# Kernel optimization log

Hardware: AMD Instinct MI355X
Metric: run time of the kernel (lower is better)

## Reference

```python
import jax, jax.numpy as jnp
import numpy as np

B, N, S, K, D = 8, 8192, 1024, 32, 64
RADIUS = 0.2
MLP = [64, 64, 128]
C_IN = 3 + D


def _fps(pts):
    # pts: [N,3] -> [S] farthest-point indices (deterministic start at index 0,
    # matching pytorch3d.sample_farthest_points default random_start_point=False)
    def body(carry, _):
        d, last = carry
        dd = jnp.sum((pts - pts[last]) ** 2, axis=-1)
        d = jnp.minimum(d, dd)
        return (d, jnp.argmax(d)), last
    init = (jnp.full((pts.shape[0],), 1e10, pts.dtype), jnp.asarray(0))
    _, idxs = jax.lax.scan(body, init, None, length=S)
    return idxs


def _ball_query(new_xyz, xyz):
    # new_xyz [B,S,3], xyz [B,N,3] -> idx [B,S,K]
    # classic PointNet++ ball query: first K points (by index order) within radius;
    # queries with fewer than K neighbors are padded by replicating the first hit.
    sqr = jnp.sum((new_xyz[:, :, None, :] - xyz[:, None, :, :]) ** 2, axis=-1)  # [B,S,N]
    cand = jnp.where(sqr <= RADIUS ** 2,
                     jnp.arange(N, dtype=jnp.int32)[None, None, :],
                     jnp.int32(N))
    idx = -jax.lax.top_k(-cand, K)[0]  # K smallest valid indices, ascending
    first = idx[..., :1]
    return jnp.where(idx == N, first, idx)


def _gather(arr, idx):
    # arr [B,N,C], idx [B,S,K] -> [B,S,K,C]
    return jax.vmap(lambda a, i: a[i])(arr, idx)


def _forward(xyz, points, attention, w0, b0, w1, b1, w2, b2):
    x = xyz.transpose(0, 2, 1)        # [B,N,3]
    p = points.transpose(0, 2, 1)     # [B,N,D]
    a = attention.transpose(0, 2, 1)  # [B,N,1]
    fps_idx = jax.vmap(_fps)(x)                      # [B,S]
    new_xyz = jax.vmap(lambda q, i: q[i])(x, fps_idx)  # [B,S,3]
    idx = _ball_query(new_xyz, x)                    # [B,S,K]
    g_norm = _gather(x, idx) - new_xyz[:, :, None, :]   # [B,S,K,3]
    feat = jnp.concatenate([g_norm, _gather(p, idx)], axis=-1)  # [B,S,K,3+D]
    new_att = jnp.mean(_gather(a, idx), axis=-2).reshape(x.shape[0], 1, -1)  # [B,1,S]
    # shared MLP (1x1 Conv2d == per-point dense), no BN (bn=False)
    h = jax.nn.relu(jnp.einsum('bskc,oc->bsko', feat, w0) + b0)
    h = jax.nn.relu(jnp.einsum('bskc,oc->bsko', h, w1) + b1)
    h = jax.nn.relu(jnp.einsum('bskc,oc->bsko', h, w2) + b2)
    new_points = jnp.max(h, axis=2)  # max-pool over nsample -> [B,S,C_out]
    return new_xyz.transpose(0, 2, 1), new_points.transpose(0, 2, 1), new_att


def setup_inputs() -> dict:
    key = jax.random.key(0)
    ks = jax.random.split(key, 9)
    xyz = jax.random.uniform(ks[0], (B, 3, N), dtype=jnp.float32)  # unit cube
    points = jax.random.normal(ks[1], (B, D, N), dtype=jnp.float32)
    attention = jax.random.uniform(ks[2], (B, 1, N), dtype=jnp.float32)
    cin = C_IN
    w0 = jax.random.normal(ks[3], (MLP[0], cin), dtype=jnp.float32) / np.sqrt(cin)
    b0 = jnp.zeros((MLP[0],), jnp.float32)
    w1 = jax.random.normal(ks[4], (MLP[1], MLP[0]), dtype=jnp.float32) / np.sqrt(MLP[0])
    b1 = jnp.zeros((MLP[1],), jnp.float32)
    w2 = jax.random.normal(ks[5], (MLP[2], MLP[1]), dtype=jnp.float32) / np.sqrt(MLP[1])
    b2 = jnp.zeros((MLP[2],), jnp.float32)
    return {"xyz": xyz, "points": points, "attention": attention,
            "w0": w0, "b0": b0, "w1": w1, "b1": b1, "w2": w2, "b2": b2}


def reference(xyz, points, attention, w0, b0, w1, b1, w2, b2):
    return _forward(xyz, points, attention, w0, b0, w1, b1, w2, b2)
```

## Files before the change

### kernel.cpp

```cpp
#include <hip/hip_runtime.h>

#define NPTS 8192
#define NSAMP 1024
#define NBATCH 8
#define KNB 32

typedef float f32x2 __attribute__((ext_vector_type(2)));

__device__ __forceinline__ f32x2 pk_add(f32x2 a, f32x2 b) {
  f32x2 d; asm("v_pk_add_f32 %0, %1, %2" : "=v"(d) : "v"(a), "v"(b)); return d;
}
__device__ __forceinline__ f32x2 pk_mul(f32x2 a, f32x2 b) {
  f32x2 d; asm("v_pk_mul_f32 %0, %1, %2" : "=v"(d) : "v"(a), "v"(b)); return d;
}

#define DPP_FMAX_ROUND(v, CTRL)                                                        \
  do {                                                                                 \
    int _b = __float_as_int(v);                                                        \
    int _p = __builtin_amdgcn_update_dpp(_b, _b, CTRL, 0xF, 0xF, false);               \
    (v) = fmaxf((v), __int_as_float(_p));                                              \
  } while (0)

#define DPP_UMIN_ROUND(v, CTRL)                                                        \
  do {                                                                                 \
    unsigned _p = (unsigned)__builtin_amdgcn_update_dpp((int)(v), (int)(v), CTRL,      \
                                                        0xF, 0xF, false);              \
    if (_p < (v)) (v) = _p;                                                            \
  } while (0)

#define DPP_MIN_ROUND(k, CTRL)                                                         \
  do {                                                                                 \
    unsigned _lo = (unsigned)(k), _hi = (unsigned)((k) >> 32);                         \
    unsigned _plo = (unsigned)__builtin_amdgcn_update_dpp((int)_lo, (int)_lo, CTRL,    \
                                                          0xF, 0xF, false);            \
    unsigned _phi = (unsigned)__builtin_amdgcn_update_dpp((int)_hi, (int)_hi, CTRL,    \
                                                          0xF, 0xF, false);            \
    unsigned long long _ok = (((unsigned long long)_phi) << 32) | _plo;                \
    if (_ok < (k)) (k) = _ok;                                                          \
  } while (0)

__device__ __forceinline__ float sqdist_rn(float px, float py, float pz,
                                           float qx, float qy, float qz) {
  float dx = px - qx, dy = py - qy, dz = pz - qz;
  return __fadd_rn(__fadd_rn(__fmul_rn(dx, dx), __fmul_rn(dy, dy)), __fmul_rn(dz, dz));
}

__global__ __launch_bounds__(512) void fps_kernel(const float* __restrict__ xyz,
                                                  float* __restrict__ out_newxyz) {
  __shared__ float cds[NPTS * 3];
  __shared__ unsigned long long wkeys[2][8];

  const int b = blockIdx.x;
  const int tid = threadIdx.x;
  const int lane = tid & 63;
  const int wv = tid >> 6;
  const float* xb = xyz + (size_t)b * 3 * NPTS;

  f32x2 X2[8], Y2[8], Z2[8], D2[8];
#pragma unroll
  for (int j = 0; j < 8; j++) {
    int n0 = tid + (2 * j) * 512, n1 = tid + (2 * j + 1) * 512;
    X2[j].x = xb[n0];            X2[j].y = xb[n1];
    Y2[j].x = xb[NPTS + n0];     Y2[j].y = xb[NPTS + n1];
    Z2[j].x = xb[2 * NPTS + n0]; Z2[j].y = xb[2 * NPTS + n1];
    D2[j].x = 1e10f;             D2[j].y = 1e10f;
    cds[n0 * 3 + 0] = X2[j].x; cds[n0 * 3 + 1] = Y2[j].x; cds[n0 * 3 + 2] = Z2[j].x;
    cds[n1 * 3 + 0] = X2[j].y; cds[n1 * 3 + 1] = Y2[j].y; cds[n1 * 3 + 2] = Z2[j].y;
  }
  __syncthreads();

  float sx = cds[0], sy = cds[1], sz = cds[2];
  unsigned c0i = 0, c1i = 0;

  for (int t = 0; t < NSAMP; t++) {
    f32x2 nqx, nqy, nqz;
    nqx.x = -sx; nqx.y = -sx;
    nqy.x = -sy; nqy.y = -sy;
    nqz.x = -sz; nqz.y = -sz;

    float bvx = -1.0f, bvy = -1.0f;
#pragma unroll
    for (int j = 0; j < 8; j++) {
      f32x2 dx = pk_add(X2[j], nqx);
      f32x2 dy = pk_add(Y2[j], nqy);
      f32x2 dz = pk_add(Z2[j], nqz);
      f32x2 dd = pk_add(pk_add(pk_mul(dx, dx), pk_mul(dy, dy)), pk_mul(dz, dz));
      float m0 = fminf(D2[j].x, dd.x);
      float m1 = fminf(D2[j].y, dd.y);
      D2[j].x = m0;
      D2[j].y = m1;
      bvx = fmaxf(bvx, m0);
      bvy = fmaxf(bvy, m1);
    }
    float bv = fmaxf(bvx, bvy);

    DPP_FMAX_ROUND(bv, 0x111);
    DPP_FMAX_ROUND(bv, 0x112);
    DPP_FMAX_ROUND(bv, 0x114);
    DPP_FMAX_ROUND(bv, 0x118);
    DPP_FMAX_ROUND(bv, 0x142);
    DPP_FMAX_ROUND(bv, 0x143);
    float wval = __int_as_float(__builtin_amdgcn_readlane(__float_as_int(bv), 63));

    int bj = 16;
#pragma unroll
    for (int j = 7; j >= 0; j--) {
      if (D2[j].y == wval) bj = 2 * j + 1;
      if (D2[j].x == wval) bj = 2 * j;
    }
    unsigned n = (unsigned)tid + ((unsigned)bj << 9);

    DPP_UMIN_ROUND(n, 0x111);
    DPP_UMIN_ROUND(n, 0x112);
    DPP_UMIN_ROUND(n, 0x114);
    DPP_UMIN_ROUND(n, 0x118);
    DPP_UMIN_ROUND(n, 0x142);
    DPP_UMIN_ROUND(n, 0x143);

    unsigned long long key =
        (((unsigned long long)(~__float_as_uint(wval))) << 32) | (unsigned long long)n;
    const int par = t & 1;
    if (lane == 63) wkeys[par][wv] = key;
    __syncthreads();
    unsigned long long k8 = wkeys[par][lane & 7];
    DPP_MIN_ROUND(k8, 0xB1);
    DPP_MIN_ROUND(k8, 0x4E);
    DPP_MIN_ROUND(k8, 0x141);
    unsigned wid = (unsigned)__builtin_amdgcn_readfirstlane((int)(unsigned)k8);

    if (t + 1 == tid) c0i = wid;
    if (t + 1 == tid + 512) c1i = wid;

    sx = cds[wid * 3 + 0];
    sy = cds[wid * 3 + 1];
    sz = cds[wid * 3 + 2];
  }

  {
    float ax = cds[c0i * 3 + 0], ay = cds[c0i * 3 + 1], az = cds[c0i * 3 + 2];
    float bx = cds[c1i * 3 + 0], by = cds[c1i * 3 + 1], bz = cds[c1i * 3 + 2];
    out_newxyz[(b * 3 + 0) * NSAMP + tid] = ax;
    out_newxyz[(b * 3 + 1) * NSAMP + tid] = ay;
    out_newxyz[(b * 3 + 2) * NSAMP + tid] = az;
    out_newxyz[(b * 3 + 0) * NSAMP + 512 + tid] = bx;
    out_newxyz[(b * 3 + 1) * NSAMP + 512 + tid] = by;
    out_newxyz[(b * 3 + 2) * NSAMP + 512 + tid] = bz;
  }
}

__global__ __launch_bounds__(256) void ballq_kernel(const float* __restrict__ xyz,
                                                    const float* __restrict__ att,
                                                    const float* __restrict__ newxyz,
                                                    int* __restrict__ idx_out,
                                                    float* __restrict__ att_out) {
  __shared__ int rowbuf[4][KNB];
  const int wv = threadIdx.x >> 6;
  const int lane = threadIdx.x & 63;
  const int g = blockIdx.x * 4 + wv;
  const int b = g >> 10;
  const int s = g & 1023;
  const float* xb = xyz + (size_t)b * 3 * NPTS;

  float qx = newxyz[(b * 3 + 0) * NSAMP + s];
  float qy = newxyz[(b * 3 + 1) * NSAMP + s];
  float qz = newxyz[(b * 3 + 2) * NSAMP + s];

  int have = 0;
  int firstn = 0;
  for (int c = 0; c < NPTS / 64; c++) {
    int n = c * 64 + lane;
    float dd = sqdist_rn(xb[n], xb[NPTS + n], xb[2 * NPTS + n], qx, qy, qz);
    bool inb = (dd <= 0.04f);
    unsigned long long m = __ballot(inb);
    if (have == 0 && m != 0ull) firstn = c * 64 + __builtin_ctzll(m);
    int pre = __popcll(m & ((1ull << lane) - 1ull));
    if (inb && (have + pre) < KNB) rowbuf[wv][have + pre] = n;
    have += __popcll(m);
    if (have >= KNB) break;
  }
  if (have > KNB) have = KNB;
  if (lane < KNB && lane >= have) rowbuf[wv][lane] = firstn;

  float av = 0.0f;
  if (lane < KNB) {
    int myidx = rowbuf[wv][lane];
    idx_out[(size_t)g * KNB + lane] = myidx;
    av = att[(size_t)b * NPTS + myidx];
  }
#pragma unroll
  for (int m = 1; m < 64; m <<= 1) av += __shfl_xor(av, m, 64);
  if (lane == 0) att_out[g] = av * 0.03125f;
}

__global__ __launch_bounds__(256) void mlp_kernel(
    const float* __restrict__ xyz, const float* __restrict__ pts,
    const float* __restrict__ newxyz, const int* __restrict__ idx,
    const float* __restrict__ w0, const float* __restrict__ b0,
    const float* __restrict__ w1, const float* __restrict__ b1,
    const float* __restrict__ w2, const float* __restrict__ b2,
    float* __restrict__ out_np) {
  const int g = blockIdx.x;
  const int b = g >> 10;
  const int s = g & 1023;
  const int t = threadIdx.x;

  __shared__ __align__(16) float feat[67 * 32];
  __shared__ __align__(16) float h0s[64 * 36];
  __shared__ __align__(16) float h1s[64 * 36];
  __shared__ int sidx[KNB];

  if (t < KNB) sidx[t] = idx[(size_t)g * KNB + t];
  __syncthreads();

  {
    int k = t & 31, rg = t >> 5;
    int n = sidx[k];
    const float* pb = pts + (size_t)b * 64 * NPTS;
    for (int r = rg; r < 67; r += 8) {
      float v;
      if (r < 3)
        v = xyz[((size_t)b * 3 + r) * NPTS + n] - newxyz[(b * 3 + r) * NSAMP + s];
      else
        v = pb[(size_t)(r - 3) * NPTS + n];
      feat[r * 32 + k] = v;
    }
  }
  __syncthreads();

  const int kq = t & 7;
  const int og = t >> 3;

  {
    float a0[8];
    float bu = b0[2 * og], bw = b0[2 * og + 1];
    a0[0] = a0[1] = a0[2] = a0[3] = bu;
    a0[4] = a0[5] = a0[6] = a0[7] = bw;
    const float* wr0 = w0 + (2 * og) * 67;
    const float* wr1 = wr0 + 67;
    for (int c = 0; c < 67; c++) {
      float4 f = *(const float4*)&feat[c * 32 + kq * 4];
      float u = wr0[c], v = wr1[c];
      a0[0] = fmaf(u, f.x, a0[0]); a0[1] = fmaf(u, f.y, a0[1]);
      a0[2] = fmaf(u, f.z, a0[2]); a0[3] = fmaf(u, f.w, a0[3]);
      a0[4] = fmaf(v, f.x, a0[4]); a0[5] = fmaf(v, f.y, a0[5]);
      a0[6] = fmaf(v, f.z, a0[6]); a0[7] = fmaf(v, f.w, a0[7]);
    }
    float4 r0, r1;
    r0.x = fmaxf(a0[0], 0.f); r0.y = fmaxf(a0[1], 0.f);
    r0.z = fmaxf(a0[2], 0.f); r0.w = fmaxf(a0[3], 0.f);
    r1.x = fmaxf(a0[4], 0.f); r1.y = fmaxf(a0[5], 0.f);
    r1.z = fmaxf(a0[6], 0.f); r1.w = fmaxf(a0[7], 0.f);
    *(float4*)&h0s[(2 * og) * 36 + kq * 4] = r0;
    *(float4*)&h0s[(2 * og + 1) * 36 + kq * 4] = r1;
  }
  __syncthreads();

  {
    float a1[8];
    float bu = b1[2 * og], bw = b1[2 * og + 1];
    a1[0] = a1[1] = a1[2] = a1[3] = bu;
    a1[4] = a1[5] = a1[6] = a1[7] = bw;
    const float* wr0 = w1 + (2 * og) * 64;
    const float* wr1 = wr0 + 64;
    for (int c = 0; c < 64; c++) {
      float4 f = *(const float4*)&h0s[c * 36 + kq * 4];
      float u = wr0[c], v = wr1[c];
      a1[0] = fmaf(u, f.x, a1[0]); a1[1] = fmaf(u, f.y, a1[1]);
      a1[2] = fmaf(u, f.z, a1[2]); a1[3] = fmaf(u, f.w, a1[3]);
      a1[4] = fmaf(v, f.x, a1[4]); a1[5] = fmaf(v, f.y, a1[5]);
      a1[6] = fmaf(v, f.z, a1[6]); a1[7] = fmaf(v, f.w, a1[7]);
    }
    float4 r0, r1;
    r0.x = fmaxf(a1[0], 0.f); r0.y = fmaxf(a1[1], 0.f);
    r0.z = fmaxf(a1[2], 0.f); r0.w = fmaxf(a1[3], 0.f);
    r1.x = fmaxf(a1[4], 0.f); r1.y = fmaxf(a1[5], 0.f);
    r1.z = fmaxf(a1[6], 0.f); r1.w = fmaxf(a1[7], 0.f);
    *(float4*)&h1s[(2 * og) * 36 + kq * 4] = r0;
    *(float4*)&h1s[(2 * og + 1) * 36 + kq * 4] = r1;
  }
  __syncthreads();

  {
    const int kq2 = t & 3;
    const int og2 = t >> 2;
    float a2[16];
    float bu = b2[2 * og2], bw = b2[2 * og2 + 1];
#pragma unroll
    for (int i = 0; i < 8; i++) { a2[i] = bu; a2[8 + i] = bw; }
    const float* wr0 = w2 + (2 * og2) * 64;
    const float* wr1 = wr0 + 64;
    for (int c = 0; c < 64; c++) {
      float4 fA = *(const float4*)&h1s[c * 36 + kq2 * 8];
      float4 fB = *(const float4*)&h1s[c * 36 + kq2 * 8 + 4];
      float u = wr0[c], v = wr1[c];
      a2[0] = fmaf(u, fA.x, a2[0]);  a2[1] = fmaf(u, fA.y, a2[1]);
      a2[2] = fmaf(u, fA.z, a2[2]);  a2[3] = fmaf(u, fA.w, a2[3]);
      a2[4] = fmaf(u, fB.x, a2[4]);  a2[5] = fmaf(u, fB.y, a2[5]);
      a2[6] = fmaf(u, fB.z, a2[6]);  a2[7] = fmaf(u, fB.w, a2[7]);
      a2[8] = fmaf(v, fA.x, a2[8]);  a2[9] = fmaf(v, fA.y, a2[9]);
      a2[10] = fmaf(v, fA.z, a2[10]); a2[11] = fmaf(v, fA.w, a2[11]);
      a2[12] = fmaf(v, fB.x, a2[12]); a2[13] = fmaf(v, fB.y, a2[13]);
      a2[14] = fmaf(v, fB.z, a2[14]); a2[15] = fmaf(v, fB.w, a2[15]);
    }
    float m0 = a2[0], m1 = a2[8];
#pragma unroll
    for (int i = 1; i < 8; i++) { m0 = fmaxf(m0, a2[i]); m1 = fmaxf(m1, a2[8 + i]); }
    m0 = fmaxf(m0, 0.f);
    m1 = fmaxf(m1, 0.f);
    m0 = fmaxf(m0, __shfl_xor(m0, 1, 64));
    m0 = fmaxf(m0, __shfl_xor(m0, 2, 64));
    m1 = fmaxf(m1, __shfl_xor(m1, 1, 64));
    m1 = fmaxf(m1, __shfl_xor(m1, 2, 64));
    if (kq2 == 0) {
      out_np[((size_t)b * 128 + 2 * og2) * NSAMP + s] = m0;
      out_np[((size_t)b * 128 + 2 * og2 + 1) * NSAMP + s] = m1;
    }
  }
}

extern "C" void kernel_launch(void* const* d_in, const int* in_sizes, int n_in,
                              void* d_out, int out_size, void* d_ws, size_t ws_size,
                              hipStream_t stream) {
  (void)in_sizes; (void)n_in; (void)out_size; (void)ws_size;
  const float* xyz = (const float*)d_in[0];
  const float* pts = (const float*)d_in[1];
  const float* att = (const float*)d_in[2];
  const float* w0 = (const float*)d_in[3];
  const float* b0 = (const float*)d_in[4];
  const float* w1 = (const float*)d_in[5];
  const float* b1 = (const float*)d_in[6];
  const float* w2 = (const float*)d_in[7];
  const float* b2 = (const float*)d_in[8];

  float* out = (float*)d_out;
  float* out_newxyz = out;
  float* out_newpts = out + NBATCH * 3 * NSAMP;
  float* out_att = out + NBATCH * 3 * NSAMP + NBATCH * 128 * NSAMP;
  int* idx_ws = (int*)d_ws;

  fps_kernel<<<NBATCH, 512, 0, stream>>>(xyz, out_newxyz);
  ballq_kernel<<<(NBATCH * NSAMP) / 4, 256, 0, stream>>>(xyz, att, out_newxyz, idx_ws, out_att);
  mlp_kernel<<<NBATCH * NSAMP, 256, 0, stream>>>(xyz, pts, out_newxyz, idx_ws,
                                                 w0, b0, w1, b1, w2, b2, out_newpts);
}
```

Baseline: 1.226 ms.

## Sort points by x in FPS and skip waves whose x-slab cannot change

Before FPS, each block bitonic-sorts its points by x coordinate in shared memory, so each wave owns a contiguous x-range. Each iteration it computes a lower bound on the squared distance from the new sample to the wave's x-slab. When that bound is not below the wave's cached max min-distance, the distance update and reductions are skipped and the cached key is reused. The cost is a full bitonic sort over 8192 points with many barriers. Per-lane argmin tie-breaking now runs on original indices.

```diff
diff --git a/kernel.cpp b/kernel.cpp
--- a/kernel.cpp
+++ b/kernel.cpp
@@ -6,6 +6,7 @@
 #define KNB 32
 
 typedef float f32x2 __attribute__((ext_vector_type(2)));
+typedef unsigned long long u64;
 
 __device__ __forceinline__ f32x2 pk_add(f32x2 a, f32x2 b) {
   f32x2 d; asm("v_pk_add_f32 %0, %1, %2" : "=v"(d) : "v"(a), "v"(b)); return d;
@@ -19,6 +20,13 @@
     int _b = __float_as_int(v);                                                        \
     int _p = __builtin_amdgcn_update_dpp(_b, _b, CTRL, 0xF, 0xF, false);               \
     (v) = fmaxf((v), __int_as_float(_p));                                              \
+  } while (0)
+
+#define DPP_FMIN_ROUND(v, CTRL)                                                        \
+  do {                                                                                 \
+    int _b = __float_as_int(v);                                                        \
+    int _p = __builtin_amdgcn_update_dpp(_b, _b, CTRL, 0xF, 0xF, false);               \
+    (v) = fminf((v), __int_as_float(_p));                                              \
   } while (0)
 
 #define DPP_UMIN_ROUND(v, CTRL)                                                        \
@@ -35,7 +43,7 @@
                                                           0xF, 0xF, false);            \
     unsigned _phi = (unsigned)__builtin_amdgcn_update_dpp((int)_hi, (int)_hi, CTRL,    \
                                                           0xF, 0xF, false);            \
-    unsigned long long _ok = (((unsigned long long)_phi) << 32) | _plo;                \
+    u64 _ok = (((u64)_phi) << 32) | _plo;                                              \
     if (_ok < (k)) (k) = _ok;                                                          \
   } while (0)
 
@@ -47,8 +55,10 @@
 
 __global__ __launch_bounds__(512) void fps_kernel(const float* __restrict__ xyz,
                                                   float* __restrict__ out_newxyz) {
-  __shared__ float cds[NPTS * 3];
-  __shared__ unsigned long long wkeys[2][8];
+  __shared__ __align__(16) char smem_raw[NPTS * 3 * 4];
+  u64* sbuf = reinterpret_cast<u64*>(smem_raw);
+  float* cds = reinterpret_cast<float*>(smem_raw);
+  __shared__ u64 wkeys[2][8];
 
   const int b = blockIdx.x;
   const int tid = threadIdx.x;
@@ -56,14 +66,59 @@
   const int wv = tid >> 6;
   const float* xb = xyz + (size_t)b * 3 * NPTS;
 
+  for (int j = 0; j < 16; j++) {
+    int n = tid + j * 512;
+    float x = xb[n];
+    sbuf[n] = (((u64)__float_as_uint(x)) << 32) | (u64)n;
+  }
+  __syncthreads();
+
+  for (unsigned k = 2; k <= (unsigned)NPTS; k <<= 1) {
+    for (unsigned jm = k >> 1; jm > 0; jm >>= 1) {
+      for (int p = 0; p < 16; p++) {
+        unsigned i = (unsigned)tid + (unsigned)p * 512u;
+        unsigned ixj = i ^ jm;
+        if (ixj > i) {
+          u64 a = sbuf[i], c = sbuf[ixj];
+          bool up = ((i & k) == 0);
+          if ((a > c) == up) { sbuf[i] = c; sbuf[ixj] = a; }
+        }
+      }
+      __syncthreads();
+    }
+  }
+
   f32x2 X2[8], Y2[8], Z2[8], D2[8];
+  unsigned idxp[8];
+  float txmin = 1e30f, txmax = -1e30f;
 #pragma unroll
   for (int j = 0; j < 8; j++) {
-    int n0 = tid + (2 * j) * 512, n1 = tid + (2 * j + 1) * 512;
-    X2[j].x = xb[n0];            X2[j].y = xb[n1];
+    u64 k0 = sbuf[tid * 16 + 2 * j];
+    u64 k1 = sbuf[tid * 16 + 2 * j + 1];
+    unsigned n0 = (unsigned)k0 & 8191u, n1 = (unsigned)k1 & 8191u;
+    float x0 = __uint_as_float((unsigned)(k0 >> 32));
+    float x1 = __uint_as_float((unsigned)(k1 >> 32));
+    X2[j].x = x0; X2[j].y = x1;
     Y2[j].x = xb[NPTS + n0];     Y2[j].y = xb[NPTS + n1];
     Z2[j].x = xb[2 * NPTS + n0]; Z2[j].y = xb[2 * NPTS + n1];
     D2[j].x = 1e10f;             D2[j].y = 1e10f;
+    idxp[j] = n0 | (n1 << 16);
+    txmin = fminf(txmin, fminf(x0, x1));
+    txmax = fmaxf(txmax, fmaxf(x0, x1));
+  }
+  DPP_FMIN_ROUND(txmin, 0x111); DPP_FMIN_ROUND(txmin, 0x112);
+  DPP_FMIN_ROUND(txmin, 0x114); DPP_FMIN_ROUND(txmin, 0x118);
+  DPP_FMIN_ROUND(txmin, 0x142); DPP_FMIN_ROUND(txmin, 0x143);
+  DPP_FMAX_ROUND(txmax, 0x111); DPP_FMAX_ROUND(txmax, 0x112);
+  DPP_FMAX_ROUND(txmax, 0x114); DPP_FMAX_ROUND(txmax, 0x118);
+  DPP_FMAX_ROUND(txmax, 0x142); DPP_FMAX_ROUND(txmax, 0x143);
+  const float xlo = __int_as_float(__builtin_amdgcn_readlane(__float_as_int(txmin), 63));
+  const float xhi = __int_as_float(__builtin_amdgcn_readlane(__float_as_int(txmax), 63));
+  __syncthreads();
+
+#pragma unroll
+  for (int j = 0; j < 8; j++) {
+    unsigned n0 = idxp[j] & 0xFFFFu, n1 = idxp[j] >> 16;
     cds[n0 * 3 + 0] = X2[j].x; cds[n0 * 3 + 1] = Y2[j].x; cds[n0 * 3 + 2] = Z2[j].x;
     cds[n1 * 3 + 0] = X2[j].y; cds[n1 * 3 + 1] = Y2[j].y; cds[n1 * 3 + 2] = Z2[j].y;
   }
@@ -71,58 +126,64 @@
 
   float sx = cds[0], sy = cds[1], sz = cds[2];
   unsigned c0i = 0, c1i = 0;
+  float bv_cache = 1e10f;
+  u64 key_cache = ~0ull;
 
   for (int t = 0; t < NSAMP; t++) {
-    f32x2 nqx, nqy, nqz;
-    nqx.x = -sx; nqx.y = -sx;
-    nqy.x = -sy; nqy.y = -sy;
-    nqz.x = -sz; nqz.y = -sz;
-
-    float bvx = -1.0f, bvy = -1.0f;
-#pragma unroll
-    for (int j = 0; j < 8; j++) {
-      f32x2 dx = pk_add(X2[j], nqx);
-      f32x2 dy = pk_add(Y2[j], nqy);
-      f32x2 dz = pk_add(Z2[j], nqz);
-      f32x2 dd = pk_add(pk_add(pk_mul(dx, dx), pk_mul(dy, dy)), pk_mul(dz, dz));
-      float m0 = fminf(D2[j].x, dd.x);
-      float m1 = fminf(D2[j].y, dd.y);
-      D2[j].x = m0;
-      D2[j].y = m1;
-      bvx = fmaxf(bvx, m0);
-      bvy = fmaxf(bvy, m1);
-    }
-    float bv = fmaxf(bvx, bvy);
-
-    DPP_FMAX_ROUND(bv, 0x111);
-    DPP_FMAX_ROUND(bv, 0x112);
-    DPP_FMAX_ROUND(bv, 0x114);
-    DPP_FMAX_ROUND(bv, 0x118);
-    DPP_FMAX_ROUND(bv, 0x142);
-    DPP_FMAX_ROUND(bv, 0x143);
-    float wval = __int_as_float(__builtin_amdgcn_readlane(__float_as_int(bv), 63));
-
-    int bj = 16;
-#pragma unroll
-    for (int j = 7; j >= 0; j--) {
-      if (D2[j].y == wval) bj = 2 * j + 1;
-      if (D2[j].x == wval) bj = 2 * j;
-    }
-    unsigned n = (unsigned)tid + ((unsigned)bj << 9);
-
-    DPP_UMIN_ROUND(n, 0x111);
-    DPP_UMIN_ROUND(n, 0x112);
-    DPP_UMIN_ROUND(n, 0x114);
-    DPP_UMIN_ROUND(n, 0x118);
-    DPP_UMIN_ROUND(n, 0x142);
-    DPP_UMIN_ROUND(n, 0x143);
-
-    unsigned long long key =
-        (((unsigned long long)(~__float_as_uint(wval))) << 32) | (unsigned long long)n;
+    float gap = fmaxf(fmaxf(xlo - sx, sx - xhi), 0.0f);
+    float lb = __fmul_rn(gap, gap);
+
+    if (lb < bv_cache) {
+      f32x2 nqx, nqy, nqz;
+      nqx.x = -sx; nqx.y = -sx;
+      nqy.x = -sy; nqy.y = -sy;
+      nqz.x = -sz; nqz.y = -sz;
+      float bvx = -1.0f, bvy = -1.0f;
+#pragma unroll
+      for (int j = 0; j < 8; j++) {
+        f32x2 dx = pk_add(X2[j], nqx);
+        f32x2 dy = pk_add(Y2[j], nqy);
+        f32x2 dz = pk_add(Z2[j], nqz);
+        f32x2 dd = pk_add(pk_add(pk_mul(dx, dx), pk_mul(dy, dy)), pk_mul(dz, dz));
+        float m0 = fminf(D2[j].x, dd.x);
+        float m1 = fminf(D2[j].y, dd.y);
+        D2[j].x = m0;
+        D2[j].y = m1;
+        bvx = fmaxf(bvx, m0);
+        bvy = fmaxf(bvy, m1);
+      }
+      float bv = fmaxf(bvx, bvy);
+
+      DPP_FMAX_ROUND(bv, 0x111);
+      DPP_FMAX_ROUND(bv, 0x112);
+      DPP_FMAX_ROUND(bv, 0x114);
+      DPP_FMAX_ROUND(bv, 0x118);
+      DPP_FMAX_ROUND(bv, 0x142);
+      DPP_FMAX_ROUND(bv, 0x143);
+      float wval = __int_as_float(__builtin_amdgcn_readlane(__float_as_int(bv), 63));
+
+      unsigned cand = 0xFFFFFFFFu;
+#pragma unroll
+      for (int j = 0; j < 8; j++) {
+        unsigned n0 = idxp[j] & 0xFFFFu, n1 = idxp[j] >> 16;
+        if (D2[j].x == wval && n0 < cand) cand = n0;
+        if (D2[j].y == wval && n1 < cand) cand = n1;
+      }
+      DPP_UMIN_ROUND(cand, 0x111);
+      DPP_UMIN_ROUND(cand, 0x112);
+      DPP_UMIN_ROUND(cand, 0x114);
+      DPP_UMIN_ROUND(cand, 0x118);
+      DPP_UMIN_ROUND(cand, 0x142);
+      DPP_UMIN_ROUND(cand, 0x143);
+
+      key_cache = (((u64)(~__float_as_uint(wval))) << 32) | (u64)cand;
+      bv_cache = wval;
+    }
+
     const int par = t & 1;
-    if (lane == 63) wkeys[par][wv] = key;
+    if (lane == 63) wkeys[par][wv] = key_cache;
     __syncthreads();
-    unsigned long long k8 = wkeys[par][lane & 7];
+    u64 k8 = wkeys[par][lane & 7];
     DPP_MIN_ROUND(k8, 0xB1);
     DPP_MIN_ROUND(k8, 0x4E);
     DPP_MIN_ROUND(k8, 0x141);
```

Result: faster. 1.160 ms (-5.3%).
